# Kernel tuning notes

Hardware: AMD Instinct MI355X
Metric: run time of the kernel (lower is better)

## Reference

```python
import jax, jax.numpy as jnp
import numpy as np

N = 100000
BN_EPS = 1e-5


def gcn_conv(x, W, b, src, dst, dinv):
    # PyG GCNConv: out = D^-1/2 (A+I) D^-1/2 (X W) + b
    h = x @ W                                   # [N, out]
    norm = dinv[src] * dinv[dst]                # [E'] edge weights
    msg = h[src] * norm[:, None]                # gather + scale  [E', out]
    agg = jax.ops.segment_sum(msg, dst, num_segments=N)
    return agg + b


def batch_norm(h, gamma, beta):
    mu = jnp.mean(h, axis=0)
    var = jnp.mean((h - mu) ** 2, axis=0)       # biased var, as torch BN training
    return gamma * (h - mu) * jax.lax.rsqrt(var + BN_EPS) + beta


def setup_inputs() -> dict:
    key = jax.random.key(0)
    ks = jax.random.split(key, 12)
    E = 1600000
    d_in, d_h, d_out = 128, 128, 40
    x = jax.random.normal(ks[0], (N, d_in), dtype=jnp.float32)
    edge_index = jax.random.randint(ks[1], (2, E), 0, N, dtype=jnp.int64)

    def glorot(k, fan_in, fan_out):
        s = jnp.sqrt(6.0 / (fan_in + fan_out))
        return jax.random.uniform(k, (fan_in, fan_out), jnp.float32, -s, s)

    return {
        "x": x,
        "W1": glorot(ks[2], d_in, d_h), "b1": jnp.zeros((d_h,), jnp.float32),
        "W2": glorot(ks[3], d_h, d_h), "b2": jnp.zeros((d_h,), jnp.float32),
        "W3": glorot(ks[4], d_h, d_out), "b3": jnp.zeros((d_out,), jnp.float32),
        "g1": 1.0 + 0.1 * jax.random.normal(ks[5], (d_h,), jnp.float32),
        "be1": 0.1 * jax.random.normal(ks[6], (d_h,), jnp.float32),
        "g2": 1.0 + 0.1 * jax.random.normal(ks[7], (d_h,), jnp.float32),
        "be2": 0.1 * jax.random.normal(ks[8], (d_h,), jnp.float32),
        "edge_index": edge_index,
    }


def reference(x, W1, b1, W2, b2, W3, b3, g1, be1, g2, be2, edge_index):
    # add self loops once (PyG add_self_loops=True)
    loop = jnp.arange(N, dtype=edge_index.dtype)
    src = jnp.concatenate([edge_index[0], loop])
    dst = jnp.concatenate([edge_index[1], loop])
    deg = jax.ops.segment_sum(jnp.ones_like(src, dtype=x.dtype), dst, num_segments=N)
    dinv = jax.lax.rsqrt(deg)                   # deg >= 1 due to self loops

    h = gcn_conv(x, W1, b1, src, dst, dinv)
    h = jax.nn.relu(batch_norm(h, g1, be1))     # dropout: identity at eval
    h = gcn_conv(h, W2, b2, src, dst, dinv)
    h = jax.nn.relu(batch_norm(h, g2, be2))
    h = gcn_conv(h, W3, b3, src, dst, dinv)
    return jax.nn.log_softmax(h, axis=1)
```

## Files before the change

### kernel.cpp

```cpp
#include <hip/hip_runtime.h>
#include <cstdint>
#include <cstddef>


typedef unsigned int uint32;
typedef __attribute__((ext_vector_type(8))) short bf16x8;
typedef __attribute__((ext_vector_type(4))) float f32x4;

__device__ inline float bl(uint32 u) { uint32 v = u << 16; return __builtin_bit_cast(float, v); }
__device__ inline float bh(uint32 u) { uint32 v = u & 0xffff0000u; return __builtin_bit_cast(float, v); }
__device__ inline uint32 f2b(float f) {
    uint32 u = __builtin_bit_cast(uint32, f);
    return (u + 0x7fffu + ((u >> 16) & 1u)) >> 16;
}
__device__ inline uint32 pack2(float x, float y) { return f2b(x) | (f2b(y) << 16); }

#define MFMA16(a, b, c) __builtin_amdgcn_mfma_f32_16x16x32_bf16(a, b, c, 0, 0, 0)
#define CSR_CH 4096
#define NSTAT 1024


__global__ __launch_bounds__(256) void bucket_hist(const int* __restrict__ dst,
                                                   int* __restrict__ bcntp,
                                                   int E, int NB) {
    __shared__ int lh[1024];
    for (int t = threadIdx.x; t < NB; t += 256) lh[t] = 0;
    __syncthreads();
    int stride = gridDim.x * 256;
    for (int e = blockIdx.x * 256 + threadIdx.x; e < E; e += stride)
        atomicAdd(&lh[dst[e] >> 7], 1);
    __syncthreads();
    for (int t = threadIdx.x; t < NB; t += 256)
        if (lh[t]) atomicAdd(&bcntp[t * 16], lh[t]);
}

__global__ __launch_bounds__(1024) void bucket_scan(const int* __restrict__ bcntp,
                                                    int* __restrict__ boffs,
                                                    int* __restrict__ bcurp, int nb) {
    __shared__ int s[1024];
    int tx = threadIdx.x;
    int v = (tx < nb) ? bcntp[tx * 16] : 0;
    s[tx] = v;
    __syncthreads();
    for (int off = 1; off < 1024; off <<= 1) {
        int t = (tx >= off) ? s[tx - off] : 0;
        __syncthreads();
        s[tx] += t;
        __syncthreads();
    }
    if (tx < nb) {
        int ex = s[tx] - v;
        boffs[tx] = ex;
        bcurp[tx * 16] = ex;
    }
    if (tx == 0) boffs[nb] = s[1023];
}

__global__ __launch_bounds__(256) void bucket_fill2(const int* __restrict__ src,
                                                    const int* __restrict__ dst,
                                                    int* __restrict__ bcurp,
                                                    uint32* __restrict__ bkt,
                                                    int E, int NB) {
    __shared__ int lh[1024];
    __shared__ int lcur[1024];
    int e0 = blockIdx.x * CSR_CH;
    int e1 = e0 + CSR_CH;
    if (e1 > E) e1 = E;
    for (int t = threadIdx.x; t < NB; t += 256) lh[t] = 0;
    __syncthreads();
    for (int e = e0 + threadIdx.x; e < e1; e += 256)
        atomicAdd(&lh[dst[e] >> 7], 1);
    __syncthreads();
    for (int t = threadIdx.x; t < NB; t += 256)
        lcur[t] = lh[t] ? atomicAdd(&bcurp[t * 16], lh[t]) : 0;
    __syncthreads();
    for (int e = e0 + threadIdx.x; e < e1; e += 256) {
        int d = dst[e];
        int b = d >> 7;
        int pos = atomicAdd(&lcur[b], 1);
        bkt[pos] = (uint32)src[e] | ((uint32)(d & 127) << 17);
    }
}

__global__ __launch_bounds__(256) void cnt_dinv(const uint32* __restrict__ bkt,
                                                const int* __restrict__ boffs,
                                                int* __restrict__ cnt,
                                                float* __restrict__ dinv, int n) {
    __shared__ int lcnt[128];
    int b = blockIdx.x;
    if (threadIdx.x < 128) lcnt[threadIdx.x] = 0;
    __syncthreads();
    int j0 = boffs[b], j1 = boffs[b + 1];
    for (int j = j0 + threadIdx.x; j < j1; j += 256)
        atomicAdd(&lcnt[bkt[j] >> 17], 1);
    __syncthreads();
    if (threadIdx.x < 128) {
        int node = b * 128 + threadIdx.x;
        if (node < n) {
            int c = lcnt[threadIdx.x];
            cnt[node] = c;
            dinv[node] = rsqrtf((float)(c + 1));
        }
    }
}

__global__ __launch_bounds__(256) void scan1(const int* __restrict__ cnt,
                                             int* __restrict__ offs,
                                             int* __restrict__ bsums, int n) {
    __shared__ int s[256];
    int tx = threadIdx.x;
    int i = blockIdx.x * 256 + tx;
    int v = (i < n) ? cnt[i] : 0;
    s[tx] = v;
    __syncthreads();
    for (int off = 1; off < 256; off <<= 1) {
        int t = (tx >= off) ? s[tx - off] : 0;
        __syncthreads();
        s[tx] += t;
        __syncthreads();
    }
    if (i < n) offs[i] = s[tx] - v;
    if (tx == 255) bsums[blockIdx.x] = s[255];
}

__global__ __launch_bounds__(512) void scan2(const int* __restrict__ bsums,
                                             int* __restrict__ bscan, int nb) {
    __shared__ int s[512];
    int tx = threadIdx.x;
    int v = (tx < nb) ? bsums[tx] : 0;
    s[tx] = v;
    __syncthreads();
    for (int off = 1; off < 512; off <<= 1) {
        int t = (tx >= off) ? s[tx - off] : 0;
        __syncthreads();
        s[tx] += t;
        __syncthreads();
    }
    if (tx < nb) bscan[tx] = s[tx] - v;
}

__global__ __launch_bounds__(256) void scan3(int* __restrict__ offs,
                                             const int* __restrict__ bscan,
                                             int n, int E) {
    int i = blockIdx.x * 256 + threadIdx.x;
    if (i < n) offs[i] += bscan[blockIdx.x];
    if (i == 0) offs[n] = E;
}

__global__ __launch_bounds__(256) void csr_fill2(const uint32* __restrict__ bkt,
                                                 const int* __restrict__ boffs,
                                                 const int* __restrict__ offs,
                                                 int* __restrict__ csr, int n) {
    __shared__ int lcur[128];
    int b = blockIdx.x;
    if (threadIdx.x < 128) {
        int node = b * 128 + threadIdx.x;
        lcur[threadIdx.x] = (node < n) ? offs[node] : 0;
    }
    __syncthreads();
    int j0 = boffs[b], j1 = boffs[b + 1];
    for (int j = j0 + threadIdx.x; j < j1; j += 256) {
        uint32 e = bkt[j];
        int dloc = e >> 17;
        int pos = atomicAdd(&lcur[dloc], 1);
        csr[pos] = (int)(e & 0x1FFFFu);
    }
}

__global__ __launch_bounds__(256) void wconv(const float* __restrict__ W1,
                                             const float* __restrict__ W2,
                                             const float* __restrict__ W3,
                                             unsigned short* __restrict__ wt1,
                                             unsigned short* __restrict__ wt2,
                                             unsigned short* __restrict__ wt3) {
    int b = blockIdx.x, tx = threadIdx.x;
    if (b < 2) {
        const float* S = b ? W2 : W1;
        unsigned short* D = b ? wt2 : wt1;
        for (int i = tx; i < 128 * 128; i += 256) {
            int k = i >> 7, nn = i & 127;
            D[nn * 128 + k] = (unsigned short)f2b(S[i]);
        }
    } else {
        for (int i = tx; i < 48 * 128; i += 256) {
            int k = i / 48, nn = i - k * 48;
            float v = (nn < 40) ? W3[k * 40 + nn] : 0.f;
            wt3[nn * 128 + k] = (unsigned short)f2b(v);
        }
    }
}


template <bool ABF16, bool BN>
__global__ __launch_bounds__(256) void gemm128m(const void* __restrict__ Av,
                                                const unsigned short* __restrict__ WT,
                                                uint32* __restrict__ C,
                                                const float* __restrict__ dinv, int n,
                                                const float* __restrict__ scale,
                                                const float* __restrict__ shift) {
    __shared__ unsigned short Wls[128 * 128];
    __shared__ unsigned short Als[128 * 128];
    int tx = threadIdx.x;
    int row0 = blockIdx.x * 128;
    {
        const uint4* srcW = (const uint4*)WT;
#pragma unroll
        for (int i = 0; i < 8; i++) {
            int cid = tx + 256 * i;
            int nr = cid >> 4, kb = cid & 15;
            uint4 u = srcW[cid];
            *(uint4*)&Wls[nr * 128 + ((kb ^ (nr & 7)) << 3)] = u;
        }
    }
    int kb = tx & 15;
    if (ABF16) {
        const uint4* src = (const uint4*)Av;
        float4 sA, sB, hA_, hB_;
        if (BN) {
            sA = ((const float4*)scale)[kb * 2];
            sB = ((const float4*)scale)[kb * 2 + 1];
            hA_ = ((const float4*)shift)[kb * 2];
            hB_ = ((const float4*)shift)[kb * 2 + 1];
        }
#pragma unroll
        for (int i = 0; i < 8; i++) {
            int r = (tx >> 4) + 16 * i;
            int gr = row0 + r;
            if (gr >= n) gr = n - 1;
            uint4 u = src[(size_t)gr * 16 + kb];
            if (BN) {
                uint4 o;
                o.x = pack2(fmaxf(0.f, bl(u.x) * sA.x + hA_.x), fmaxf(0.f, bh(u.x) * sA.y + hA_.y));
                o.y = pack2(fmaxf(0.f, bl(u.y) * sA.z + hA_.z), fmaxf(0.f, bh(u.y) * sA.w + hA_.w));
                o.z = pack2(fmaxf(0.f, bl(u.z) * sB.x + hB_.x), fmaxf(0.f, bh(u.z) * sB.y + hB_.y));
                o.w = pack2(fmaxf(0.f, bl(u.w) * sB.z + hB_.z), fmaxf(0.f, bh(u.w) * sB.w + hB_.w));
                u = o;
            }
            *(uint4*)&Als[r * 128 + ((kb ^ (r & 7)) << 3)] = u;
        }
    } else {
        const float4* src = (const float4*)Av;
#pragma unroll
        for (int i = 0; i < 8; i++) {
            int r = (tx >> 4) + 16 * i;
            int gr = row0 + r;
            if (gr >= n) gr = n - 1;
            float4 a = src[(size_t)gr * 32 + kb * 2];
            float4 b = src[(size_t)gr * 32 + kb * 2 + 1];
            uint4 u;
            u.x = pack2(a.x, a.y);
            u.y = pack2(a.z, a.w);
            u.z = pack2(b.x, b.y);
            u.w = pack2(b.z, b.w);
            *(uint4*)&Als[r * 128 + ((kb ^ (r & 7)) << 3)] = u;
        }
    }
    __syncthreads();

    int w = tx >> 6, lane = tx & 63;
    int r0 = w * 32;
    int lrow = lane & 15, lkg = lane >> 4;
    f32x4 acc[2][8];
#pragma unroll
    for (int rt = 0; rt < 2; rt++)
#pragma unroll
        for (int nt = 0; nt < 8; nt++) acc[rt][nt] = (f32x4){0.f, 0.f, 0.f, 0.f};
#pragma unroll
    for (int ks = 0; ks < 4; ks++) {
        int kbl = ks * 4 + lkg;
        int r = r0 + lrow;
        bf16x8 a0 = *(const bf16x8*)&Als[r * 128 + ((kbl ^ (r & 7)) << 3)];
        int r2 = r0 + 16 + lrow;
        bf16x8 a1 = *(const bf16x8*)&Als[r2 * 128 + ((kbl ^ (r2 & 7)) << 3)];
#pragma unroll
        for (int nt = 0; nt < 8; nt++) {
            int nr = nt * 16 + lrow;
            bf16x8 b = *(const bf16x8*)&Wls[nr * 128 + ((kbl ^ (nr & 7)) << 3)];
            acc[0][nt] = MFMA16(a0, b, acc[0][nt]);
            acc[1][nt] = MFMA16(a1, b, acc[1][nt]);
        }
    }
    float* SL = (float*)&Als[w * 4096];
#pragma unroll
    for (int rt = 0; rt < 2; rt++) {
#pragma unroll
        for (int nt = 0; nt < 8; nt++)
#pragma unroll
            for (int j = 0; j < 4; j++)
                SL[(lkg * 4 + j) * 128 + nt * 16 + lrow] = acc[rt][nt][j];
#pragma unroll
        for (int i = 0; i < 8; i++) {
            int rloc = i * 2 + (lane >> 5);
            int gr = row0 + r0 + rt * 16 + rloc;
            int cq = lane & 31;
            if (gr < n) {
                float dv = dinv[gr];
                float4 v = *(float4*)&SL[rloc * 128 + cq * 4];
                uint2 o;
                o.x = pack2(v.x * dv, v.y * dv);
                o.y = pack2(v.z * dv, v.w * dv);
                *(uint2*)&C[(size_t)gr * 64 + cq * 2] = o;
            }
        }
        if (rt == 0) __builtin_amdgcn_s_waitcnt(0);
    }
}

__global__ __launch_bounds__(256) void gemm40m(const uint32* __restrict__ A,
                                               const unsigned short* __restrict__ WT,
                                               unsigned short* __restrict__ C,
                                               const float* __restrict__ dinv, int n,
                                               const float* __restrict__ scale,
                                               const float* __restrict__ shift) {
    __shared__ unsigned short Wls[48 * 128];
    __shared__ unsigned short Als[128 * 128];
    int tx = threadIdx.x;
    int row0 = blockIdx.x * 128;
    {
        const uint4* srcW = (const uint4*)WT;
#pragma unroll
        for (int i = 0; i < 3; i++) {
            int cid = tx + 256 * i;
            int nr = cid >> 4, kb = cid & 15;
            uint4 u = srcW[cid];
            *(uint4*)&Wls[nr * 128 + ((kb ^ (nr & 7)) << 3)] = u;
        }
    }
    int kb = tx & 15;
    {
        const uint4* src = (const uint4*)A;
        float4 sA = ((const float4*)scale)[kb * 2];
        float4 sB = ((const float4*)scale)[kb * 2 + 1];
        float4 hA_ = ((const float4*)shift)[kb * 2];
        float4 hB_ = ((const float4*)shift)[kb * 2 + 1];
#pragma unroll
        for (int i = 0; i < 8; i++) {
            int r = (tx >> 4) + 16 * i;
            int gr = row0 + r;
            if (gr >= n) gr = n - 1;
            uint4 u = src[(size_t)gr * 16 + kb];
            uint4 o;
            o.x = pack2(fmaxf(0.f, bl(u.x) * sA.x + hA_.x), fmaxf(0.f, bh(u.x) * sA.y + hA_.y));
            o.y = pack2(fmaxf(0.f, bl(u.y) * sA.z + hA_.z), fmaxf(0.f, bh(u.y) * sA.w + hA_.w));
            o.z = pack2(fmaxf(0.f, bl(u.z) * sB.x + hB_.x), fmaxf(0.f, bh(u.z) * sB.y + hB_.y));
            o.w = pack2(fmaxf(0.f, bl(u.w) * sB.z + hB_.z), fmaxf(0.f, bh(u.w) * sB.w + hB_.w));
            *(uint4*)&Als[r * 128 + ((kb ^ (r & 7)) << 3)] = o;
        }
    }
    __syncthreads();

    int w = tx >> 6, lane = tx & 63;
    int r0 = w * 32;
    int lrow = lane & 15, lkg = lane >> 4;
    f32x4 acc[2][3];
#pragma unroll
    for (int rt = 0; rt < 2; rt++)
#pragma unroll
        for (int nt = 0; nt < 3; nt++) acc[rt][nt] = (f32x4){0.f, 0.f, 0.f, 0.f};
#pragma unroll
    for (int ks = 0; ks < 4; ks++) {
        int kbl = ks * 4 + lkg;
        int r = r0 + lrow;
        bf16x8 a0 = *(const bf16x8*)&Als[r * 128 + ((kbl ^ (r & 7)) << 3)];
        int r2 = r0 + 16 + lrow;
        bf16x8 a1 = *(const bf16x8*)&Als[r2 * 128 + ((kbl ^ (r2 & 7)) << 3)];
#pragma unroll
        for (int nt = 0; nt < 3; nt++) {
            int nr = nt * 16 + lrow;
            bf16x8 b = *(const bf16x8*)&Wls[nr * 128 + ((kbl ^ (nr & 7)) << 3)];
            acc[0][nt] = MFMA16(a0, b, acc[0][nt]);
            acc[1][nt] = MFMA16(a1, b, acc[1][nt]);
        }
    }
#pragma unroll
    for (int rt = 0; rt < 2; rt++)
#pragma unroll
        for (int j = 0; j < 4; j++) {
            int gr = row0 + r0 + rt * 16 + lkg * 4 + j;
            if (gr < n) {
                float dv = dinv[gr];
#pragma unroll
                for (int nt = 0; nt < 3; nt++) {
                    int col = nt * 16 + lrow;
                    if (col < 40)
                        C[(size_t)gr * 40 + col] = (unsigned short)f2b(acc[rt][nt][j] * dv);
                }
            }
        }
}


__global__ __launch_bounds__(256) void agg128(const uint32* __restrict__ h,
                                              const int* __restrict__ csr,
                                              const int* __restrict__ offs,
                                              const float* __restrict__ dinv,
                                              const float* __restrict__ bias,
                                              uint32* __restrict__ out, int n) {
    int wid = (blockIdx.x * 256 + threadIdx.x) >> 6;
    int lane = threadIdx.x & 63;
    if (wid >= n) return;
    uint32 self = h[(size_t)wid * 64 + lane];
    float ax0 = bl(self), ay0 = bh(self);
    float ax1 = 0.f, ay1 = 0.f;
    int e0 = offs[wid], e1 = offs[wid + 1];
    int e = e0;
    while (e < e1) {
        int cnt = e1 - e;
        if (cnt > 64) cnt = 64;
        int sl = (lane < cnt) ? csr[e + lane] : 0;
        int j = 0;
        for (; j + 3 < cnt; j += 4) {
            int s0 = __shfl(sl, j, 64);
            int s1 = __shfl(sl, j + 1, 64);
            int s2 = __shfl(sl, j + 2, 64);
            int s3 = __shfl(sl, j + 3, 64);
            uint32 u0 = h[(size_t)s0 * 64 + lane];
            uint32 u1 = h[(size_t)s1 * 64 + lane];
            uint32 u2 = h[(size_t)s2 * 64 + lane];
            uint32 u3 = h[(size_t)s3 * 64 + lane];
            ax0 += bl(u0); ay0 += bh(u0);
            ax1 += bl(u1); ay1 += bh(u1);
            ax0 += bl(u2); ay0 += bh(u2);
            ax1 += bl(u3); ay1 += bh(u3);
        }
        for (; j < cnt; j++) {
            int s = __shfl(sl, j, 64);
            uint32 u = h[(size_t)s * 64 + lane];
            ax0 += bl(u); ay0 += bh(u);
        }
        e += cnt;
    }
    float ax = ax0 + ax1, ay = ay0 + ay1;
    float di = dinv[wid];
    float2 b = ((const float2*)bias)[lane];
    out[(size_t)wid * 64 + lane] = pack2(ax * di + b.x, ay * di + b.y);
}

__global__ __launch_bounds__(256) void agg40_lsm(const uint32* __restrict__ h,
                                                 const int* __restrict__ csr,
                                                 const int* __restrict__ offs,
                                                 const float* __restrict__ dinv,
                                                 const float* __restrict__ bias,
                                                 float* __restrict__ out, int n) {
    int wid = (blockIdx.x * 256 + threadIdx.x) >> 6;
    int lane = threadIdx.x & 63;
    if (wid >= n) return;
    int grp = lane / 20;
    int c = lane - grp * 20;
    bool work = grp < 3;
    float vx = 0.f, vy = 0.f;
    if (grp == 0) {
        uint32 u = h[(size_t)wid * 20 + c];
        vx = bl(u);
        vy = bh(u);
    }
    int e0 = offs[wid], e1 = offs[wid + 1];
    int e = e0;
    while (e < e1) {
        int cnt = e1 - e;
        if (cnt > 64) cnt = 64;
        int sl = (lane < cnt) ? csr[e + lane] : 0;
        int nIt = (cnt + 5) / 6;
        for (int it = 0; it < nIt; it++) {
            int j0 = it * 6 + grp;
            int j1 = j0 + 3;
            int s0 = __shfl(sl, (j0 < cnt) ? j0 : 0, 64);
            int s1 = __shfl(sl, (j1 < cnt) ? j1 : 0, 64);
            if (work && j0 < cnt) {
                uint32 u = h[(size_t)s0 * 20 + c];
                vx += bl(u); vy += bh(u);
            }
            if (work && j1 < cnt) {
                uint32 u = h[(size_t)s1 * 20 + c];
                vx += bl(u); vy += bh(u);
            }
        }
        e += cnt;
    }
    float t1x = __shfl(vx, (lane + 20) & 63, 64), t2x = __shfl(vx, (lane + 40) & 63, 64);
    float t1y = __shfl(vy, (lane + 20) & 63, 64), t2y = __shfl(vy, (lane + 40) & 63, 64);
    vx += t1x + t2x;
    vy += t1y + t2y;
    float di = dinv[wid];
    float v0 = -1e30f, v1 = -1e30f;
    if (lane < 20) {
        v0 = vx * di + bias[2 * lane];
        v1 = vy * di + bias[2 * lane + 1];
    }
    float m = fmaxf(v0, v1);
    for (int off = 16; off; off >>= 1) m = fmaxf(m, __shfl_xor(m, off, 64));
    float ss = (lane < 20) ? (expf(v0 - m) + expf(v1 - m)) : 0.f;
    for (int off = 16; off; off >>= 1) ss += __shfl_xor(ss, off, 64);
    float lg = logf(ss);
    if (lane < 20) {
        float2 o;
        o.x = v0 - m - lg;
        o.y = v1 - m - lg;
        ((float2*)out)[(size_t)wid * 20 + lane] = o;
    }
}


__global__ __launch_bounds__(256) void stats_k(const uint32* __restrict__ h,
                                               float* __restrict__ psum,
                                               float* __restrict__ psq, int n) {
    int kb = threadIdx.x & 15;
    int rg = threadIdx.x >> 4;
    float s[8], q[8];
#pragma unroll
    for (int j = 0; j < 8; j++) { s[j] = 0.f; q[j] = 0.f; }
    const uint4* h4 = (const uint4*)h;
    for (int r = blockIdx.x * 16 + rg; r < n; r += gridDim.x * 16) {
        uint4 u = h4[(size_t)r * 16 + kb];
        float f[8] = {bl(u.x), bh(u.x), bl(u.y), bh(u.y),
                      bl(u.z), bh(u.z), bl(u.w), bh(u.w)};
#pragma unroll
        for (int j = 0; j < 8; j++) { s[j] += f[j]; q[j] += f[j] * f[j]; }
    }
    __shared__ float LS[16][16][8];
    __shared__ float LQ[16][16][8];
#pragma unroll
    for (int j = 0; j < 8; j++) { LS[rg][kb][j] = s[j]; LQ[rg][kb][j] = q[j]; }
    __syncthreads();
    if (threadIdx.x < 128) {
        int cq = threadIdx.x >> 3, j = threadIdx.x & 7;
        float S = 0.f, Q = 0.f;
#pragma unroll
        for (int g = 0; g < 16; g++) { S += LS[g][cq][j]; Q += LQ[g][cq][j]; }
        psum[blockIdx.x * 128 + cq * 8 + j] = S;
        psq[blockIdx.x * 128 + cq * 8 + j] = Q;
    }
}

__global__ __launch_bounds__(1024) void finalize_stats(const float* __restrict__ psum,
                                                       const float* __restrict__ psq,
                                                       const float* __restrict__ g,
                                                       const float* __restrict__ be,
                                                       float* __restrict__ scale,
                                                       float* __restrict__ shift,
                                                       int nb, float invN) {
    int c = threadIdx.x & 127;
    int seg = threadIdx.x >> 7;
    int per = nb >> 3;
    float s = 0.f, q = 0.f;
    for (int b = seg * per; b < (seg + 1) * per; b++) {
        s += psum[b * 128 + c];
        q += psq[b * 128 + c];
    }
    __shared__ float LS[8][128], LQ[8][128];
    LS[seg][c] = s;
    LQ[seg][c] = q;
    __syncthreads();
    if (threadIdx.x < 128) {
        float S = 0.f, Q = 0.f;
#pragma unroll
        for (int g2 = 0; g2 < 8; g2++) { S += LS[g2][c]; Q += LQ[g2][c]; }
        float mu = S * invN;
        float var = Q * invN - mu * mu;
        float sc = g[c] * rsqrtf(var + 1e-5f);
        scale[c] = sc;
        shift[c] = be[c] - mu * sc;
    }
}

extern "C" void kernel_launch(void* const* d_in, const int* in_sizes, int n_in,
                              void* d_out, int out_size, void* d_ws, size_t ws_size,
                              hipStream_t stream) {
    const float* x   = (const float*)d_in[0];
    const float* W1  = (const float*)d_in[1];
    const float* b1  = (const float*)d_in[2];
    const float* W2  = (const float*)d_in[3];
    const float* b2  = (const float*)d_in[4];
    const float* W3  = (const float*)d_in[5];
    const float* b3  = (const float*)d_in[6];
    const float* g1  = (const float*)d_in[7];
    const float* be1 = (const float*)d_in[8];
    const float* g2  = (const float*)d_in[9];
    const float* be2 = (const float*)d_in[10];
    const int*   ei  = (const int*)d_in[11];

    int n = in_sizes[0] / 128;
    int E = in_sizes[11] / 2;
    const int* src = ei;
    const int* dst = ei + E;
    int NB = (n + 127) >> 7;

    char* p = (char*)d_ws;
    size_t off = 0;
    auto alloc = [&](size_t bytes) -> void* {
        off = (off + 255) & ~(size_t)255;
        void* r = p + off;
        off += bytes;
        return r;
    };
    uint32* hA    = (uint32*)alloc((size_t)n * 64 * 4);
    uint32* hB    = (uint32*)alloc((size_t)n * 64 * 4);
    float* dinv   = (float*)alloc((size_t)n * 4);
    int*   cnt    = (int*)alloc((size_t)n * 4);
    int*   offs   = (int*)alloc((size_t)(n + 1) * 4);
    int*   bsums  = (int*)alloc(512 * 4);
    int*   bscan  = (int*)alloc(512 * 4);
    int*   csr    = (int*)alloc((size_t)E * 4);
    float* psum   = (float*)alloc((size_t)NSTAT * 128 * 4);
    float* psq    = (float*)alloc((size_t)NSTAT * 128 * 4);
    float* scale  = (float*)alloc(128 * 4);
    float* shift  = (float*)alloc(128 * 4);
    unsigned short* wt1 = (unsigned short*)alloc(128 * 128 * 2);
    unsigned short* wt2 = (unsigned short*)alloc(128 * 128 * 2);
    unsigned short* wt3 = (unsigned short*)alloc(48 * 128 * 2);
    int*   bcntp  = (int*)alloc((size_t)NB * 16 * 4);
    int*   boffs  = (int*)alloc((size_t)(NB + 1) * 4);
    int*   bcurp  = (int*)alloc((size_t)NB * 16 * 4);
    uint32* bkt   = hA;
    (void)ws_size;

    int nbN = (n + 255) / 256;
    int gG = (n + 127) / 128;
    int gAgg = (n * 64 + 255) / 256;
    int gFill = (E + CSR_CH - 1) / CSR_CH;
    float invN = 1.0f / (float)n;

    hipMemsetAsync(bcntp, 0, (size_t)NB * 16 * 4, stream);

    wconv<<<3, 256, 0, stream>>>(W1, W2, W3, wt1, wt2, wt3);
    bucket_hist<<<256, 256, 0, stream>>>(dst, bcntp, E, NB);
    bucket_scan<<<1, 1024, 0, stream>>>(bcntp, boffs, bcurp, NB);
    bucket_fill2<<<gFill, 256, 0, stream>>>(src, dst, bcurp, bkt, E, NB);
    cnt_dinv<<<NB, 256, 0, stream>>>(bkt, boffs, cnt, dinv, n);
    scan1<<<nbN, 256, 0, stream>>>(cnt, offs, bsums, n);
    scan2<<<1, 512, 0, stream>>>(bsums, bscan, nbN);
    scan3<<<nbN, 256, 0, stream>>>(offs, bscan, n, E);
    csr_fill2<<<NB, 256, 0, stream>>>(bkt, boffs, offs, csr, n);

    gemm128m<false, false><<<gG, 256, 0, stream>>>(x, wt1, hA, dinv, n, nullptr, nullptr);
    agg128<<<gAgg, 256, 0, stream>>>(hA, csr, offs, dinv, b1, hB, n);
    stats_k<<<NSTAT, 256, 0, stream>>>(hB, psum, psq, n);
    finalize_stats<<<1, 1024, 0, stream>>>(psum, psq, g1, be1, scale, shift, NSTAT, invN);

    gemm128m<true, true><<<gG, 256, 0, stream>>>(hB, wt2, hA, dinv, n, scale, shift);
    agg128<<<gAgg, 256, 0, stream>>>(hA, csr, offs, dinv, b2, hB, n);
    stats_k<<<NSTAT, 256, 0, stream>>>(hB, psum, psq, n);
    finalize_stats<<<1, 1024, 0, stream>>>(psum, psq, g2, be2, scale, shift, NSTAT, invN);

    gemm40m<<<gG, 256, 0, stream>>>(hB, wt3, (unsigned short*)hA, dinv, n, scale, shift);
    agg40_lsm<<<gAgg, 256, 0, stream>>>(hA, csr, offs, dinv, b3, (float*)d_out, n);
}
```

Measured before the change: 426.9 us.

## Fuse CSR build into one bucket kernel and widen aggregation gathers

Replaces the cnt_dinv, three-kernel global scan and csr_fill2 chain with a single per-bucket kernel. It derives node offsets from the bucket offsets plus a local 128-entry scan, then fills CSR in the same pass, removing four launches and a global prefix sum. The agg128 and agg40_lsm kernels now gather 8-byte (uint2) rows, with each half-wave or lane group handling a different neighbor, followed by cross-lane reductions. This trades extra shuffle reductions for fewer and wider memory requests per edge.

```diff
diff --git a/kernel.cpp b/kernel.cpp
--- a/kernel.cpp
+++ b/kernel.cpp
@@ -82,84 +82,43 @@
     }
 }
 
-__global__ __launch_bounds__(256) void cnt_dinv(const uint32* __restrict__ bkt,
-                                                const int* __restrict__ boffs,
-                                                int* __restrict__ cnt,
-                                                float* __restrict__ dinv, int n) {
+__global__ __launch_bounds__(256) void bucket_csr(const uint32* __restrict__ bkt,
+                                                  const int* __restrict__ boffs,
+                                                  float* __restrict__ dinv,
+                                                  int* __restrict__ offs,
+                                                  int* __restrict__ csr, int n) {
     __shared__ int lcnt[128];
-    int b = blockIdx.x;
-    if (threadIdx.x < 128) lcnt[threadIdx.x] = 0;
-    __syncthreads();
-    int j0 = boffs[b], j1 = boffs[b + 1];
-    for (int j = j0 + threadIdx.x; j < j1; j += 256)
-        atomicAdd(&lcnt[bkt[j] >> 17], 1);
-    __syncthreads();
-    if (threadIdx.x < 128) {
-        int node = b * 128 + threadIdx.x;
-        if (node < n) {
-            int c = lcnt[threadIdx.x];
-            cnt[node] = c;
-            dinv[node] = rsqrtf((float)(c + 1));
-        }
-    }
-}
-
-__global__ __launch_bounds__(256) void scan1(const int* __restrict__ cnt,
-                                             int* __restrict__ offs,
-                                             int* __restrict__ bsums, int n) {
-    __shared__ int s[256];
-    int tx = threadIdx.x;
-    int i = blockIdx.x * 256 + tx;
-    int v = (i < n) ? cnt[i] : 0;
-    s[tx] = v;
-    __syncthreads();
-    for (int off = 1; off < 256; off <<= 1) {
-        int t = (tx >= off) ? s[tx - off] : 0;
-        __syncthreads();
-        s[tx] += t;
-        __syncthreads();
-    }
-    if (i < n) offs[i] = s[tx] - v;
-    if (tx == 255) bsums[blockIdx.x] = s[255];
-}
-
-__global__ __launch_bounds__(512) void scan2(const int* __restrict__ bsums,
-                                             int* __restrict__ bscan, int nb) {
-    __shared__ int s[512];
-    int tx = threadIdx.x;
-    int v = (tx < nb) ? bsums[tx] : 0;
-    s[tx] = v;
-    __syncthreads();
-    for (int off = 1; off < 512; off <<= 1) {
-        int t = (tx >= off) ? s[tx - off] : 0;
-        __syncthreads();
-        s[tx] += t;
-        __syncthreads();
-    }
-    if (tx < nb) bscan[tx] = s[tx] - v;
-}
-
-__global__ __launch_bounds__(256) void scan3(int* __restrict__ offs,
-                                             const int* __restrict__ bscan,
-                                             int n, int E) {
-    int i = blockIdx.x * 256 + threadIdx.x;
-    if (i < n) offs[i] += bscan[blockIdx.x];
-    if (i == 0) offs[n] = E;
-}
-
-__global__ __launch_bounds__(256) void csr_fill2(const uint32* __restrict__ bkt,
-                                                 const int* __restrict__ boffs,
-                                                 const int* __restrict__ offs,
-                                                 int* __restrict__ csr, int n) {
+    __shared__ int lscan[128];
     __shared__ int lcur[128];
     int b = blockIdx.x;
-    if (threadIdx.x < 128) {
-        int node = b * 128 + threadIdx.x;
-        lcur[threadIdx.x] = (node < n) ? offs[node] : 0;
-    }
+    int tx = threadIdx.x;
+    if (tx < 128) lcnt[tx] = 0;
     __syncthreads();
     int j0 = boffs[b], j1 = boffs[b + 1];
-    for (int j = j0 + threadIdx.x; j < j1; j += 256) {
+    for (int j = j0 + tx; j < j1; j += 256)
+        atomicAdd(&lcnt[bkt[j] >> 17], 1);
+    __syncthreads();
+    if (tx < 128) lscan[tx] = lcnt[tx];
+    __syncthreads();
+    for (int off = 1; off < 128; off <<= 1) {
+        int v = 0;
+        if (tx < 128 && tx >= off) v = lscan[tx - off];
+        __syncthreads();
+        if (tx < 128) lscan[tx] += v;
+        __syncthreads();
+    }
+    if (tx < 128) {
+        int node = b * 128 + tx;
+        if (node < n) {
+            int o = j0 + lscan[tx] - lcnt[tx];
+            offs[node] = o;
+            lcur[tx] = o;
+            dinv[node] = rsqrtf((float)(lcnt[tx] + 1));
+        }
+    }
+    if (b == gridDim.x - 1 && tx == 0) offs[n] = j1;
+    __syncthreads();
+    for (int j = j0 + tx; j < j1; j += 256) {
         uint32 e = bkt[j];
         int dloc = e >> 17;
         int pos = atomicAdd(&lcur[dloc], 1);
@@ -399,9 +358,15 @@
     int wid = (blockIdx.x * 256 + threadIdx.x) >> 6;
     int lane = threadIdx.x & 63;
     if (wid >= n) return;
-    uint32 self = h[(size_t)wid * 64 + lane];
-    float ax0 = bl(self), ay0 = bh(self);
-    float ax1 = 0.f, ay1 = 0.f;
+    int half = lane >> 5;
+    int t = lane & 31;
+    const uint2* h2 = (const uint2*)h;
+    float a0 = 0.f, a1 = 0.f, a2 = 0.f, a3 = 0.f;
+    float c0 = 0.f, c1 = 0.f, c2 = 0.f, c3 = 0.f;
+    if (half == 0) {
+        uint2 u = h2[(size_t)wid * 32 + t];
+        a0 = bl(u.x); a1 = bh(u.x); a2 = bl(u.y); a3 = bh(u.y);
+    }
     int e0 = offs[wid], e1 = offs[wid + 1];
     int e = e0;
     while (e < e1) {
@@ -410,30 +375,35 @@
         int sl = (lane < cnt) ? csr[e + lane] : 0;
         int j = 0;
         for (; j + 3 < cnt; j += 4) {
-            int s0 = __shfl(sl, j, 64);
-            int s1 = __shfl(sl, j + 1, 64);
-            int s2 = __shfl(sl, j + 2, 64);
-            int s3 = __shfl(sl, j + 3, 64);
-            uint32 u0 = h[(size_t)s0 * 64 + lane];
-            uint32 u1 = h[(size_t)s1 * 64 + lane];
-            uint32 u2 = h[(size_t)s2 * 64 + lane];
-            uint32 u3 = h[(size_t)s3 * 64 + lane];
-            ax0 += bl(u0); ay0 += bh(u0);
-            ax1 += bl(u1); ay1 += bh(u1);
-            ax0 += bl(u2); ay0 += bh(u2);
-            ax1 += bl(u3); ay1 += bh(u3);
+            int sa = __shfl(sl, j + half, 64);
+            int sb = __shfl(sl, j + 2 + half, 64);
+            uint2 ua = h2[(size_t)sa * 32 + t];
+            uint2 ub = h2[(size_t)sb * 32 + t];
+            a0 += bl(ua.x); a1 += bh(ua.x); a2 += bl(ua.y); a3 += bh(ua.y);
+            c0 += bl(ub.x); c1 += bh(ub.x); c2 += bl(ub.y); c3 += bh(ub.y);
         }
         for (; j < cnt; j++) {
             int s = __shfl(sl, j, 64);
-            uint32 u = h[(size_t)s * 64 + lane];
-            ax0 += bl(u); ay0 += bh(u);
+            if (half == (j & 1)) {
+                uint2 u = h2[(size_t)s * 32 + t];
+                a0 += bl(u.x); a1 += bh(u.x); a2 += bl(u.y); a3 += bh(u.y);
+            }
         }
         e += cnt;
     }
-    float ax = ax0 + ax1, ay = ay0 + ay1;
-    float di = dinv[wid];
-    float2 b = ((const float2*)bias)[lane];
-    out[(size_t)wid * 64 + lane] = pack2(ax * di + b.x, ay * di + b.y);
+    a0 += c0; a1 += c1; a2 += c2; a3 += c3;
+    a0 += __shfl_xor(a0, 32, 64);
+    a1 += __shfl_xor(a1, 32, 64);
+    a2 += __shfl_xor(a2, 32, 64);
+    a3 += __shfl_xor(a3, 32, 64);
+    if (half == 0) {
+        float di = dinv[wid];
+        float4 bb = ((const float4*)bias)[t];
+        uint2 o;
+        o.x = pack2(a0 * di + bb.x, a1 * di + bb.y);
+        o.y = pack2(a2 * di + bb.z, a3 * di + bb.w);
+        ((uint2*)out)[(size_t)wid * 32 + t] = o;
+    }
 }
 
 __global__ __launch_bounds__(256) void agg40_lsm(const uint32* __restrict__ h,
@@ -445,14 +415,14 @@
     int wid = (blockIdx.x * 256 + threadIdx.x) >> 6;
     int lane = threadIdx.x & 63;
     if (wid >= n) return;
-    int grp = lane / 20;
-    int c = lane - grp * 20;
-    bool work = grp < 3;
-    float vx = 0.f, vy = 0.f;
+    int grp = lane / 10;
+    int t = lane - grp * 10;
+    bool work = grp < 6;
+    const uint2* h2 = (const uint2*)h;
+    float a0 = 0.f, a1 = 0.f, a2 = 0.f, a3 = 0.f;
     if (grp == 0) {
-        uint32 u = h[(size_t)wid * 20 + c];
-        vx = bl(u);
-        vy = bh(u);
+        uint2 u = h2[(size_t)wid * 10 + t];
+        a0 = bl(u.x); a1 = bh(u.x); a2 = bl(u.y); a3 = bh(u.y);
     }
     int e0 = offs[wid], e1 = offs[wid + 1];
     int e = e0;
@@ -460,43 +430,52 @@
         int cnt = e1 - e;
         if (cnt > 64) cnt = 64;
         int sl = (lane < cnt) ? csr[e + lane] : 0;
-        int nIt = (cnt + 5) / 6;
+        int nIt = (cnt + 11) / 12;
         for (int it = 0; it < nIt; it++) {
-            int j0 = it * 6 + grp;
-            int j1 = j0 + 3;
+            int j0 = it * 12 + grp;
+            int j1 = j0 + 6;
             int s0 = __shfl(sl, (j0 < cnt) ? j0 : 0, 64);
             int s1 = __shfl(sl, (j1 < cnt) ? j1 : 0, 64);
             if (work && j0 < cnt) {
-                uint32 u = h[(size_t)s0 * 20 + c];
-                vx += bl(u); vy += bh(u);
+                uint2 u = h2[(size_t)s0 * 10 + t];
+                a0 += bl(u.x); a1 += bh(u.x); a2 += bl(u.y); a3 += bh(u.y);
             }
             if (work && j1 < cnt) {
-                uint32 u = h[(size_t)s1 * 20 + c];
-                vx += bl(u); vy += bh(u);
+                uint2 u = h2[(size_t)s1 * 10 + t];
+                a0 += bl(u.x); a1 += bh(u.x); a2 += bl(u.y); a3 += bh(u.y);
             }
         }
         e += cnt;
     }
-    float t1x = __shfl(vx, (lane + 20) & 63, 64), t2x = __shfl(vx, (lane + 40) & 63, 64);
-    float t1y = __shfl(vy, (lane + 20) & 63, 64), t2y = __shfl(vy, (lane + 40) & 63, 64);
-    vx += t1x + t2x;
-    vy += t1y + t2y;
+    a0 += __shfl(a0, (lane + 30) & 63, 64);
+    a1 += __shfl(a1, (lane + 30) & 63, 64);
+    a2 += __shfl(a2, (lane + 30) & 63, 64);
+    a3 += __shfl(a3, (lane + 30) & 63, 64);
+    {
+        float t0 = __shfl(a0, (lane + 10) & 63, 64), u0 = __shfl(a0, (lane + 20) & 63, 64);
+        float t1 = __shfl(a1, (lane + 10) & 63, 64), u1 = __shfl(a1, (lane + 20) & 63, 64);
+        float t2 = __shfl(a2, (lane + 10) & 63, 64), u2 = __shfl(a2, (lane + 20) & 63, 64);
+        float t3 = __shfl(a3, (lane + 10) & 63, 64), u3 = __shfl(a3, (lane + 20) & 63, 64);
+        a0 += t0 + u0; a1 += t1 + u1; a2 += t2 + u2; a3 += t3 + u3;
+    }
+    bool act = lane < 10;
     float di = dinv[wid];
-    float v0 = -1e30f, v1 = -1e30f;
-    if (lane < 20) {
-        v0 = vx * di + bias[2 * lane];
-        v1 = vy * di + bias[2 * lane + 1];
-    }
-    float m = fmaxf(v0, v1);
-    for (int off = 16; off; off >>= 1) m = fmaxf(m, __shfl_xor(m, off, 64));
-    float ss = (lane < 20) ? (expf(v0 - m) + expf(v1 - m)) : 0.f;
-    for (int off = 16; off; off >>= 1) ss += __shfl_xor(ss, off, 64);
+    float v0 = -1e30f, v1 = -1e30f, v2 = -1e30f, v3 = -1e30f;
+    if (act) {
+        float4 bb = ((const float4*)bias)[t];
+        v0 = a0 * di + bb.x;
+        v1 = a1 * di + bb.y;
+        v2 = a2 * di + bb.z;
+        v3 = a3 * di + bb.w;
+    }
+    float m = fmaxf(fmaxf(v0, v1), fmaxf(v2, v3));
+    for (int off = 8; off; off >>= 1) m = fmaxf(m, __shfl_xor(m, off, 64));
+    float ss = act ? (expf(v0 - m) + expf(v1 - m) + expf(v2 - m) + expf(v3 - m)) : 0.f;
+    for (int off = 8; off; off >>= 1) ss += __shfl_xor(ss, off, 64);
     float lg = logf(ss);
-    if (lane < 20) {
-        float2 o;
-        o.x = v0 - m - lg;
-        o.y = v1 - m - lg;
-        ((float2*)out)[(size_t)wid * 20 + lane] = o;
+    if (act) {
+        float4 o = {v0 - m - lg, v1 - m - lg, v2 - m - lg, v3 - m - lg};
+        *(float4*)&out[(size_t)wid * 40 + t * 4] = o;
     }
 }
 
@@ -596,10 +575,7 @@
     uint32* hA    = (uint32*)alloc((size_t)n * 64 * 4);
     uint32* hB    = (uint32*)alloc((size_t)n * 64 * 4);
     float* dinv   = (float*)alloc((size_t)n * 4);
-    int*   cnt    = (int*)alloc((size_t)n * 4);
     int*   offs   = (int*)alloc((size_t)(n + 1) * 4);
-    int*   bsums  = (int*)alloc(512 * 4);
-    int*   bscan  = (int*)alloc(512 * 4);
     int*   csr    = (int*)alloc((size_t)E * 4);
     float* psum   = (float*)alloc((size_t)NSTAT * 128 * 4);
     float* psq    = (float*)alloc((size_t)NSTAT * 128 * 4);
@@ -614,7 +590,6 @@
     uint32* bkt   = hA;
     (void)ws_size;
 
-    int nbN = (n + 255) / 256;
     int gG = (n + 127) / 128;
     int gAgg = (n * 64 + 255) / 256;
     int gFill = (E + CSR_CH - 1) / CSR_CH;
@@ -626,11 +601,7 @@
     bucket_hist<<<256, 256, 0, stream>>>(dst, bcntp, E, NB);
     bucket_scan<<<1, 1024, 0, stream>>>(bcntp, boffs, bcurp, NB);
     bucket_fill2<<<gFill, 256, 0, stream>>>(src, dst, bcurp, bkt, E, NB);
-    cnt_dinv<<<NB, 256, 0, stream>>>(bkt, boffs, cnt, dinv, n);
-    scan1<<<nbN, 256, 0, stream>>>(cnt, offs, bsums, n);
-    scan2<<<1, 512, 0, stream>>>(bsums, bscan, nbN);
-    scan3<<<nbN, 256, 0, stream>>>(offs, bscan, n, E);
-    csr_fill2<<<NB, 256, 0, stream>>>(bkt, boffs, offs, csr, n);
+    bucket_csr<<<NB, 256, 0, stream>>>(bkt, boffs, dinv, offs, csr, n);
 
     gemm128m<false, false><<<gG, 256, 0, stream>>>(x, wt1, hA, dinv, n, nullptr, nullptr);
     agg128<<<gAgg, 256, 0, stream>>>(hA, csr, offs, dinv, b1, hB, n);
```

After: 429.5 us. About the same (+0.6%).
